# Kernel tuning notes

Measured on AMD Instinct MI355X. Metric: run time of the kernel, lower is better.

The kernel has to match this reference:

```python
import jax, jax.numpy as jnp
import numpy as np

N = 100000
F_IN = 128
HID = 64
N_CLS = 40
E = 1600000


def gcn_conv(x, src, dst, W, b, n_nodes):
    """PyG GCNConv: add self-loops, symmetric deg^{-1/2} normalization.

    Self-loop contribution handled analytically (norm_ii = 1/deg_i) so we
    never concatenate self-loop edges.
    """
    h = x @ W                                      # [N, out]
    # in-degree including self-loop
    deg = jax.ops.segment_sum(jnp.ones((src.shape[0],), x.dtype), dst,
                              num_segments=n_nodes) + 1.0
    dinv = jax.lax.rsqrt(deg)                      # deg^{-1/2}, [N]
    norm = dinv[src] * dinv[dst]                   # [E]
    msg = h[src] * norm[:, None]                   # [E, out] gather + scale
    agg = jax.ops.segment_sum(msg, dst, num_segments=n_nodes)
    return agg + h * (dinv * dinv)[:, None] + b


def setup_inputs() -> dict:
    key = jax.random.key(0)
    k1, k2, k3, k4, k5, k6 = jax.random.split(key, 6)
    x = jax.random.normal(k1, (N, F_IN), dtype=jnp.float32)
    edge_index = jax.random.randint(k2, (2, E), 0, N, dtype=jnp.int64)
    W1 = jax.random.normal(k3, (F_IN, HID), dtype=jnp.float32) / np.sqrt(F_IN)
    b1 = jnp.zeros((HID,), jnp.float32)
    W2 = jax.random.normal(k4, (HID, N_CLS), dtype=jnp.float32) / np.sqrt(HID)
    b2 = jnp.zeros((N_CLS,), jnp.float32)
    return {"x": x, "edge_index": edge_index, "W1": W1, "b1": b1,
            "W2": W2, "b2": b2}


def reference(x, edge_index, W1, b1, W2, b2):
    src, dst = edge_index[0], edge_index[1]
    h = jax.nn.relu(gcn_conv(x, src, dst, W1, b1, N))
    # dropout p=0.5 is identity at inference (training=False)
    out = gcn_conv(h, src, dst, W2, b2, N)
    return out
```

## Files before the change

kernel.cpp:

```cpp
#include <hip/hip_runtime.h>
#include <stdint.h>

#define NN    100000
#define FIN   128
#define HIDN  64
#define NCLS  40
#define NE    1600000
#define NBUCK ((NN + 255) / 256)
#define EPB   4096
#define NEB   ((NE + EPB - 1) / EPB)

typedef unsigned int uint32;
typedef __attribute__((ext_vector_type(8))) short short8v;
typedef __attribute__((ext_vector_type(4))) float f32x4;

static __device__ __forceinline__ unsigned short f2bf(float f) {
  uint32 u = __float_as_uint(f);
  u = (u + 0x7fffu + ((u >> 16) & 1u)) >> 16;
  return (unsigned short)u;
}
static __device__ __forceinline__ uint32 pack2(float lo, float hi) {
  return (uint32)f2bf(lo) | ((uint32)f2bf(hi) << 16);
}
static __device__ __forceinline__ float bf_lo(uint32 v) {
  return __uint_as_float(v << 16);
}
static __device__ __forceinline__ float bf_hi(uint32 v) {
  return __uint_as_float(v & 0xFFFF0000u);
}
static __device__ __forceinline__ f32x4 mfma_bf16(uint4 a, uint4 b, f32x4 c) {
  short8v av = __builtin_bit_cast(short8v, a);
  short8v bv = __builtin_bit_cast(short8v, b);
  return __builtin_amdgcn_mfma_f32_16x16x32_bf16(av, bv, c, 0, 0, 0);
}

static __device__ __forceinline__ int perm_col(int z) {
  return 4 * (z >> 3) + ((z & 7) >> 1) + 16 * (z & 1) + ((z >= 32) ? 16 : 0);
}

__global__ __launch_bounds__(64) void probe_kernel(const unsigned int* __restrict__ raw,
                                                   int* __restrict__ flag) {
  if (threadIdx.x == 0) {
    int is64 = 1;
    for (int i = 0; i < 64; ++i)
      if (raw[2 * i + 1] != 0u) { is64 = 0; break; }
    *flag = is64;
  }
}

__global__ __launch_bounds__(64) void wfrag_kernel(const float* __restrict__ W,
                                                   const float* __restrict__ b1,
                                                   uint4* __restrict__ wfrag,
                                                   float* __restrict__ b1p) {
  int idx = blockIdx.x * 64 + threadIdx.x;
  if (idx < 64) b1p[idx] = b1[perm_col(idx)];
  int lane = idx & 63;
  int nr = (idx >> 6) & 3;
  int kr = (idx >> 8) & 3;
  int t  = idx >> 10;
  int n  = nr * 16 + (lane & 15);
  int k0 = kr * 32 + (lane >> 4) * 8;
  uint32 w[4];
#pragma unroll
  for (int j = 0; j < 4; ++j) {
    float a = W[(k0 + 2 * j) * HIDN + n];
    float b = W[(k0 + 2 * j + 1) * HIDN + n];
    uint32 ha = f2bf(a), hb = f2bf(b);
    if (t == 0) {
      w[j] = ha | (hb << 16);
    } else {
      float ra = a - __uint_as_float(ha << 16);
      float rb = b - __uint_as_float(hb << 16);
      w[j] = (uint32)f2bf(ra) | ((uint32)f2bf(rb) << 16);
    }
  }
  wfrag[idx] = make_uint4(w[0], w[1], w[2], w[3]);
}

__global__ __launch_bounds__(256) void passA_kernel(const void* __restrict__ eptr,
                                                    const int* __restrict__ flag,
                                                    int* __restrict__ mat) {
  __shared__ int cnt[NBUCK];
  int tid = threadIdx.x;
  for (int i = tid; i < NBUCK; i += 256) cnt[i] = 0;
  __syncthreads();
  int is64 = *flag;
  int base = blockIdx.x * EPB;
#pragma unroll
  for (int k = 0; k < EPB / 256; ++k) {
    int e = base + k * 256 + tid;
    if (e < NE) {
      int d = is64 ? (int)((const long long*)eptr)[e + NE]
                   : ((const int*)eptr)[e + NE];
      atomicAdd(&cnt[d >> 8], 1);
    }
  }
  __syncthreads();
  for (int i = tid; i < NBUCK; i += 256)
    mat[blockIdx.x * NBUCK + i] = cnt[i];
}

__global__ __launch_bounds__(512) void passB1_kernel(int* __restrict__ mat,
                                                     int* __restrict__ tot) {
  __shared__ int s[512];
  int b = blockIdx.x;
  int t = threadIdx.x;
  int v = (t < NEB) ? mat[t * NBUCK + b] : 0;
  s[t] = v;
  __syncthreads();
#pragma unroll
  for (int d = 1; d < 512; d <<= 1) {
    int u = (t >= d) ? s[t - d] : 0;
    __syncthreads();
    s[t] += u;
    __syncthreads();
  }
  if (t < NEB) mat[t * NBUCK + b] = s[t] - v;
  if (t == 511) tot[b] = s[511];
}

__global__ __launch_bounds__(512) void passB2_kernel(const int* __restrict__ tot,
                                                     int* __restrict__ bbase) {
  __shared__ int s[512];
  int i = threadIdx.x;
  int v = (i < NBUCK) ? tot[i] : 0;
  s[i] = v;
  __syncthreads();
#pragma unroll
  for (int d = 1; d < 512; d <<= 1) {
    int u = (i >= d) ? s[i - d] : 0;
    __syncthreads();
    s[i] += u;
    __syncthreads();
  }
  if (i < NBUCK) bbase[i] = s[i] - v;
  if (i == 511) bbase[NBUCK] = s[511];
}

__global__ __launch_bounds__(256) void passC_kernel(const void* __restrict__ eptr,
                                                    const int* __restrict__ flag,
                                                    const int* __restrict__ mat,
                                                    const int* __restrict__ bbase,
                                                    uint32* __restrict__ bbuf) {
  __shared__ int cur[NBUCK];
  int tid = threadIdx.x;
  for (int i = tid; i < NBUCK; i += 256)
    cur[i] = bbase[i] + mat[blockIdx.x * NBUCK + i];
  __syncthreads();
  int is64 = *flag;
  int base = blockIdx.x * EPB;
#pragma unroll
  for (int k = 0; k < EPB / 256; ++k) {
    int e = base + k * 256 + tid;
    if (e < NE) {
      int s, d;
      if (is64) {
        const long long* p = (const long long*)eptr;
        s = (int)p[e]; d = (int)p[e + NE];
      } else {
        const int* p = (const int*)eptr;
        s = p[e]; d = p[e + NE];
      }
      int slot = atomicAdd(&cur[d >> 8], 1);
      bbuf[slot] = (uint32)s | ((uint32)(d & 255) << 17);
    }
  }
}

__global__ __launch_bounds__(256) void build_kernel(const int* __restrict__ bbase,
                                                    const uint32* __restrict__ bbuf,
                                                    int* __restrict__ off,
                                                    float* __restrict__ dinv,
                                                    int* __restrict__ s_src) {
  __shared__ int hist[256];
  __shared__ int lofs[256];
  __shared__ int rank[256];
  int b = blockIdx.x, tid = threadIdx.x;
  int base = bbase[b];
  int count = bbase[b + 1] - base;
  const uint32* p = bbuf + base;
  hist[tid] = 0;
  __syncthreads();
  for (int i = tid; i < count; i += 256) atomicAdd(&hist[p[i] >> 17], 1);
  __syncthreads();
  int deg = hist[tid];
  lofs[tid] = deg;
  __syncthreads();
#pragma unroll
  for (int dd = 1; dd < 256; dd <<= 1) {
    int t = (tid >= dd) ? lofs[tid - dd] : 0;
    __syncthreads();
    lofs[tid] += t;
    __syncthreads();
  }
  int excl = lofs[tid] - deg;
  __syncthreads();
  lofs[tid] = excl;
  rank[tid] = 0;
  int n = b * 256 + tid;
  if (n < NN) {
    off[n] = base + excl;
    dinv[n] = rsqrtf((float)deg + 1.0f);
  }
  if (b == 0 && tid == 0) off[NN] = NE;
  __syncthreads();
  for (int i = tid; i < count; i += 256) {
    uint32 v = p[i];
    int dl = (int)(v >> 17);
    int s = (int)(v & 0x1FFFFu);
    int r = atomicAdd(&rank[dl], 1);
    s_src[base + lofs[dl] + r] = s;
  }
}

__global__ __launch_bounds__(256) void gemm1_kernel(const float* __restrict__ x,
                                                    const uint4* __restrict__ wfrag,
                                                    const float* __restrict__ dinv,
                                                    uint32* __restrict__ hs) {
  int wid = blockIdx.x * 4 + (threadIdx.x >> 6);
  if (wid >= NN / 32) return;
  int lane = threadIdx.x & 63;
  int l15 = lane & 15, lg = lane >> 4;
  int r0 = wid * 32;
  f32x4 acc[2][4];
#pragma unroll
  for (int mr = 0; mr < 2; ++mr)
#pragma unroll
    for (int nr = 0; nr < 4; ++nr) acc[mr][nr] = (f32x4)0.f;
  const float4* x4 = (const float4*)x;
#pragma unroll
  for (int kr = 0; kr < 4; ++kr) {
    uint4 ah[2], al[2];
#pragma unroll
    for (int mr = 0; mr < 2; ++mr) {
      int m = r0 + mr * 16 + l15;
      int q0 = m * 32 + kr * 8 + lg * 2;
      float4 u = x4[q0], v = x4[q0 + 1];
      float xs[8] = {u.x, u.y, u.z, u.w, v.x, v.y, v.z, v.w};
      uint32 hw[4], lw[4];
#pragma unroll
      for (int j = 0; j < 4; ++j) {
        float a0 = xs[2 * j], a1 = xs[2 * j + 1];
        uint32 h0 = f2bf(a0), h1 = f2bf(a1);
        float ra = a0 - __uint_as_float(h0 << 16);
        float rb = a1 - __uint_as_float(h1 << 16);
        hw[j] = h0 | (h1 << 16);
        lw[j] = (uint32)f2bf(ra) | ((uint32)f2bf(rb) << 16);
      }
      ah[mr] = make_uint4(hw[0], hw[1], hw[2], hw[3]);
      al[mr] = make_uint4(lw[0], lw[1], lw[2], lw[3]);
    }
#pragma unroll
    for (int nr = 0; nr < 4; ++nr) {
      uint4 bh = wfrag[(kr * 4 + nr) * 64 + lane];
      uint4 bl = wfrag[((4 + kr) * 4 + nr) * 64 + lane];
#pragma unroll
      for (int mr = 0; mr < 2; ++mr) {
        acc[mr][nr] = mfma_bf16(ah[mr], bh, acc[mr][nr]);
        acc[mr][nr] = mfma_bf16(al[mr], bh, acc[mr][nr]);
        acc[mr][nr] = mfma_bf16(ah[mr], bl, acc[mr][nr]);
      }
    }
  }
#pragma unroll
  for (int mr = 0; mr < 2; ++mr) {
    int rb = r0 + mr * 16 + 4 * lg;
    float4 dv = *(const float4*)&dinv[rb];
#pragma unroll
    for (int a = 0; a < 2; ++a) {
#pragma unroll
      for (int j = 0; j < 4; ++j) {
        float d = (&dv.x)[j];
        uint32 wv = pack2(acc[mr][2 * a][j] * d, acc[mr][2 * a + 1][j] * d);
        hs[(size_t)(rb + j) * 32 + a * 16 + l15] = wv;
      }
    }
  }
}

__global__ __launch_bounds__(256) void agg1_kernel(const int* __restrict__ off,
                                                   const int* __restrict__ s_src,
                                                   const uint4* __restrict__ hs4,
                                                   const float* __restrict__ dinv,
                                                   const float* __restrict__ b1p,
                                                   uint4* __restrict__ g) {
  int tid = threadIdx.x;
  int n = blockIdx.x * 32 + (tid >> 3);
  int hc = tid & 7;
  int j0 = off[n], j1 = off[n + 1];
  float a[8];
  {
    uint4 v = hs4[(size_t)n * 8 + hc];
    a[0] = bf_lo(v.x); a[1] = bf_hi(v.x); a[2] = bf_lo(v.y); a[3] = bf_hi(v.y);
    a[4] = bf_lo(v.z); a[5] = bf_hi(v.z); a[6] = bf_lo(v.w); a[7] = bf_hi(v.w);
  }
  int j = j0;
  for (; j + 1 < j1; j += 2) {
    int sa = s_src[j], sb = s_src[j + 1];
    uint4 va = hs4[(size_t)sa * 8 + hc];
    uint4 vb = hs4[(size_t)sb * 8 + hc];
    a[0] += bf_lo(va.x); a[1] += bf_hi(va.x); a[2] += bf_lo(va.y); a[3] += bf_hi(va.y);
    a[4] += bf_lo(va.z); a[5] += bf_hi(va.z); a[6] += bf_lo(va.w); a[7] += bf_hi(va.w);
    a[0] += bf_lo(vb.x); a[1] += bf_hi(vb.x); a[2] += bf_lo(vb.y); a[3] += bf_hi(vb.y);
    a[4] += bf_lo(vb.z); a[5] += bf_hi(vb.z); a[6] += bf_lo(vb.w); a[7] += bf_hi(vb.w);
  }
  if (j < j1) {
    int sa = s_src[j];
    uint4 va = hs4[(size_t)sa * 8 + hc];
    a[0] += bf_lo(va.x); a[1] += bf_hi(va.x); a[2] += bf_lo(va.y); a[3] += bf_hi(va.y);
    a[4] += bf_lo(va.z); a[5] += bf_hi(va.z); a[6] += bf_lo(va.w); a[7] += bf_hi(va.w);
  }
  float di = dinv[n];
  float4 b0 = *(const float4*)&b1p[hc * 8];
  float4 b4 = *(const float4*)&b1p[hc * 8 + 4];
  float r0 = di * fmaxf(a[0] * di + b0.x, 0.f);
  float r1 = di * fmaxf(a[1] * di + b0.y, 0.f);
  float r2 = di * fmaxf(a[2] * di + b0.z, 0.f);
  float r3 = di * fmaxf(a[3] * di + b0.w, 0.f);
  float r4 = di * fmaxf(a[4] * di + b4.x, 0.f);
  float r5 = di * fmaxf(a[5] * di + b4.y, 0.f);
  float r6 = di * fmaxf(a[6] * di + b4.z, 0.f);
  float r7 = di * fmaxf(a[7] * di + b4.w, 0.f);
  uint4 o;
  o.x = pack2(r0, r1); o.y = pack2(r2, r3);
  o.z = pack2(r4, r5); o.w = pack2(r6, r7);
  g[(size_t)n * 8 + hc] = o;
}

__global__ __launch_bounds__(256) void agg2_kernel(const int* __restrict__ off,
                                                   const int* __restrict__ s_src,
                                                   const uint4* __restrict__ g,
                                                   const float* __restrict__ dinv,
                                                   float* __restrict__ t) {
  int tid = threadIdx.x;
  int n = blockIdx.x * 32 + (tid >> 3);
  int hc = tid & 7;
  int j0 = off[n], j1 = off[n + 1];
  float a[8];
  {
    uint4 v = g[(size_t)n * 8 + hc];
    a[0] = bf_lo(v.x); a[1] = bf_hi(v.x); a[2] = bf_lo(v.y); a[3] = bf_hi(v.y);
    a[4] = bf_lo(v.z); a[5] = bf_hi(v.z); a[6] = bf_lo(v.w); a[7] = bf_hi(v.w);
  }
  int j = j0;
  for (; j + 1 < j1; j += 2) {
    int sa = s_src[j], sb = s_src[j + 1];
    uint4 va = g[(size_t)sa * 8 + hc];
    uint4 vb = g[(size_t)sb * 8 + hc];
    a[0] += bf_lo(va.x); a[1] += bf_hi(va.x); a[2] += bf_lo(va.y); a[3] += bf_hi(va.y);
    a[4] += bf_lo(va.z); a[5] += bf_hi(va.z); a[6] += bf_lo(va.w); a[7] += bf_hi(va.w);
    a[0] += bf_lo(vb.x); a[1] += bf_hi(vb.x); a[2] += bf_lo(vb.y); a[3] += bf_hi(vb.y);
    a[4] += bf_lo(vb.z); a[5] += bf_hi(vb.z); a[6] += bf_lo(vb.w); a[7] += bf_hi(vb.w);
  }
  if (j < j1) {
    int sa = s_src[j];
    uint4 va = g[(size_t)sa * 8 + hc];
    a[0] += bf_lo(va.x); a[1] += bf_hi(va.x); a[2] += bf_lo(va.y); a[3] += bf_hi(va.y);
    a[4] += bf_lo(va.z); a[5] += bf_hi(va.z); a[6] += bf_lo(va.w); a[7] += bf_hi(va.w);
  }
  float di = dinv[n];
  float* tp = &t[(size_t)n * HIDN + hc * 8];
  *(float4*)tp = make_float4(a[0] * di, a[1] * di, a[2] * di, a[3] * di);
  *(float4*)(tp + 4) = make_float4(a[4] * di, a[5] * di, a[6] * di, a[7] * di);
}

__global__ __launch_bounds__(256) void mv_kernel(const float* __restrict__ t,
                                                 const float* __restrict__ W2,
                                                 const float* __restrict__ b2,
                                                 float* __restrict__ out) {
  __shared__ float sW[HIDN * NCLS];
  int tid = threadIdx.x;
  for (int i = tid; i < HIDN * (NCLS / 4); i += 256) {
    int z = i / 10, j = i - z * 10;
    int c = perm_col(z);
    ((float4*)sW)[z * 10 + j] = ((const float4*)W2)[c * 10 + j];
  }
  __syncthreads();
  int cg = tid & 1;
  int r = blockIdx.x * 128 + (tid >> 1);
  if (r >= NN) return;
  int c0 = cg * 20;
  float acc[20];
#pragma unroll
  for (int j = 0; j < 20; ++j) acc[j] = b2[c0 + j];
  const float4* t4 = (const float4*)(t + (size_t)r * HIDN);
#pragma unroll 4
  for (int k4 = 0; k4 < 16; ++k4) {
    float4 tv = t4[k4];
#pragma unroll
    for (int kk = 0; kk < 4; ++kk) {
      float xv = (&tv.x)[kk];
      const float* wr = &sW[(k4 * 4 + kk) * NCLS + c0];
#pragma unroll
      for (int j = 0; j < 5; ++j) {
        float4 wv = *(const float4*)&wr[j * 4];
        acc[j * 4 + 0] = fmaf(xv, wv.x, acc[j * 4 + 0]);
        acc[j * 4 + 1] = fmaf(xv, wv.y, acc[j * 4 + 1]);
        acc[j * 4 + 2] = fmaf(xv, wv.z, acc[j * 4 + 2]);
        acc[j * 4 + 3] = fmaf(xv, wv.w, acc[j * 4 + 3]);
      }
    }
  }
  float4* op = (float4*)&out[(size_t)r * NCLS + c0];
#pragma unroll
  for (int j = 0; j < 5; ++j)
    op[j] = make_float4(acc[j * 4 + 0], acc[j * 4 + 1],
                        acc[j * 4 + 2], acc[j * 4 + 3]);
}

extern "C" void kernel_launch(void* const* d_in, const int* in_sizes, int n_in,
                              void* d_out, int out_size, void* d_ws, size_t ws_size,
                              hipStream_t stream) {
  const float* x  = (const float*)d_in[0];
  const void*  ei = d_in[1];
  const float* W1 = (const float*)d_in[2];
  const float* b1 = (const float*)d_in[3];
  const float* W2 = (const float*)d_in[4];
  const float* b2 = (const float*)d_in[5];
  float* out = (float*)d_out;

  char* w = (char*)d_ws;
  size_t off_b = 0;
  auto carve = [&](size_t bytes) -> void* {
    void* p = w + off_b;
    off_b = (off_b + bytes + 255) & ~(size_t)255;
    return p;
  };
  int*    mat   = (int*)   carve((size_t)NEB * NBUCK * 4);
  int*    tot   = (int*)   carve((size_t)NBUCK * 4);
  int*    bbase = (int*)   carve((size_t)(NBUCK + 1) * 4);
  int*    offs  = (int*)   carve((size_t)(NN + 1) * 4);
  float*  dinv  = (float*) carve((size_t)NN * 4);
  int*    flag  = (int*)   carve(256);
  int*    s_src = (int*)   carve((size_t)NE * 4);
  uint32* hs    = (uint32*)carve((size_t)NN * 32 * 4);
  uint4*  g     = (uint4*) carve((size_t)NN * 8 * 16);
  float*  t     = (float*) carve((size_t)NN * HIDN * 4);
  uint32* bbuf  = (uint32*)carve((size_t)NE * 4);
  uint4*  wfrag = (uint4*) carve((size_t)2048 * 16);
  float*  b1p   = (float*) carve((size_t)HIDN * 4);

  probe_kernel<<<1, 64, 0, stream>>>((const unsigned int*)ei, flag);
  wfrag_kernel<<<32, 64, 0, stream>>>(W1, b1, wfrag, b1p);
  passA_kernel<<<NEB, 256, 0, stream>>>(ei, flag, mat);
  passB1_kernel<<<NBUCK, 512, 0, stream>>>(mat, tot);
  passB2_kernel<<<1, 512, 0, stream>>>(tot, bbase);
  passC_kernel<<<NEB, 256, 0, stream>>>(ei, flag, mat, bbase, bbuf);
  build_kernel<<<NBUCK, 256, 0, stream>>>(bbase, bbuf, offs, dinv, s_src);
  gemm1_kernel<<<(NN / 32 + 3) / 4, 256, 0, stream>>>(x, wfrag, dinv, hs);
  agg1_kernel<<<NN / 32, 256, 0, stream>>>(offs, s_src, (const uint4*)hs, dinv, b1p, g);
  agg2_kernel<<<NN / 32, 256, 0, stream>>>(offs, s_src, g, dinv, t);
  mv_kernel<<<(NN + 127) / 128, 256, 0, stream>>>(t, W2, b2, out);
}
```

Measured before the change: 247.1 us.

## Fuse second aggregation with W2 matvec via LDS and unroll gathers by four

Merges the layer-2 aggregation and the final 64x40 matvec into one kernel. Each block stages its 32 aggregated rows in shared memory, then every thread computes 5 output classes using a transposed, column-permuted W2 that is prepared once in the weight prep kernel. This removes the fp32 intermediate t round trip through global memory (about 25.6 MB written and read) and one launch. Both aggregation loops now unroll neighbor gathers by four to keep more loads in flight. The trade-off is that W2 is read from global/L2 per thread rather than from LDS, and output stores are scalar and strided.

New measurement: 334.7 us. 35.4% more time.

```diff
diff --git a/kernel.cpp b/kernel.cpp
--- a/kernel.cpp
+++ b/kernel.cpp
@@ -38,6 +38,14 @@
   return 4 * (z >> 3) + ((z & 7) >> 1) + 16 * (z & 1) + ((z >= 32) ? 16 : 0);
 }
 
+#define ACC8(v)                                                              \
+  do {                                                                       \
+    a[0] += bf_lo((v).x); a[1] += bf_hi((v).x);                              \
+    a[2] += bf_lo((v).y); a[3] += bf_hi((v).y);                              \
+    a[4] += bf_lo((v).z); a[5] += bf_hi((v).z);                              \
+    a[6] += bf_lo((v).w); a[7] += bf_hi((v).w);                              \
+  } while (0)
+
 __global__ __launch_bounds__(64) void probe_kernel(const unsigned int* __restrict__ raw,
                                                    int* __restrict__ flag) {
   if (threadIdx.x == 0) {
@@ -50,10 +58,16 @@
 
 __global__ __launch_bounds__(64) void wfrag_kernel(const float* __restrict__ W,
                                                    const float* __restrict__ b1,
+                                                   const float* __restrict__ W2,
                                                    uint4* __restrict__ wfrag,
-                                                   float* __restrict__ b1p) {
+                                                   float* __restrict__ b1p,
+                                                   float* __restrict__ W2pc) {
   int idx = blockIdx.x * 64 + threadIdx.x;
   if (idx < 64) b1p[idx] = b1[perm_col(idx)];
+  for (int i = idx; i < HIDN * NCLS; i += 2048) {
+    int c = i >> 6, z = i & 63;
+    W2pc[i] = W2[perm_col(z) * NCLS + c];
+  }
   int lane = idx & 63;
   int nr = (idx >> 6) & 3;
   int kr = (idx >> 8) & 3;
@@ -295,20 +309,17 @@
     a[4] = bf_lo(v.z); a[5] = bf_hi(v.z); a[6] = bf_lo(v.w); a[7] = bf_hi(v.w);
   }
   int j = j0;
-  for (; j + 1 < j1; j += 2) {
-    int sa = s_src[j], sb = s_src[j + 1];
-    uint4 va = hs4[(size_t)sa * 8 + hc];
-    uint4 vb = hs4[(size_t)sb * 8 + hc];
-    a[0] += bf_lo(va.x); a[1] += bf_hi(va.x); a[2] += bf_lo(va.y); a[3] += bf_hi(va.y);
-    a[4] += bf_lo(va.z); a[5] += bf_hi(va.z); a[6] += bf_lo(va.w); a[7] += bf_hi(va.w);
-    a[0] += bf_lo(vb.x); a[1] += bf_hi(vb.x); a[2] += bf_lo(vb.y); a[3] += bf_hi(vb.y);
-    a[4] += bf_lo(vb.z); a[5] += bf_hi(vb.z); a[6] += bf_lo(vb.w); a[7] += bf_hi(vb.w);
-  }
-  if (j < j1) {
-    int sa = s_src[j];
-    uint4 va = hs4[(size_t)sa * 8 + hc];
-    a[0] += bf_lo(va.x); a[1] += bf_hi(va.x); a[2] += bf_lo(va.y); a[3] += bf_hi(va.y);
-    a[4] += bf_lo(va.z); a[5] += bf_hi(va.z); a[6] += bf_lo(va.w); a[7] += bf_hi(va.w);
+  for (; j + 3 < j1; j += 4) {
+    int s0 = s_src[j], s1 = s_src[j + 1], s2 = s_src[j + 2], s3 = s_src[j + 3];
+    uint4 v0 = hs4[(size_t)s0 * 8 + hc];
+    uint4 v1 = hs4[(size_t)s1 * 8 + hc];
+    uint4 v2 = hs4[(size_t)s2 * 8 + hc];
+    uint4 v3 = hs4[(size_t)s3 * 8 + hc];
+    ACC8(v0); ACC8(v1); ACC8(v2); ACC8(v3);
+  }
+  for (; j < j1; ++j) {
+    uint4 v0 = hs4[(size_t)s_src[j] * 8 + hc];
+    ACC8(v0);
   }
   float di = dinv[n];
   float4 b0 = *(const float4*)&b1p[hc * 8];
@@ -327,13 +338,17 @@
   g[(size_t)n * 8 + hc] = o;
 }
 
-__global__ __launch_bounds__(256) void agg2_kernel(const int* __restrict__ off,
-                                                   const int* __restrict__ s_src,
-                                                   const uint4* __restrict__ g,
-                                                   const float* __restrict__ dinv,
-                                                   float* __restrict__ t) {
+__global__ __launch_bounds__(256) void agg2mv_kernel(const int* __restrict__ off,
+                                                     const int* __restrict__ s_src,
+                                                     const uint4* __restrict__ g,
+                                                     const float* __restrict__ dinv,
+                                                     const float* __restrict__ W2pc,
+                                                     const float* __restrict__ b2,
+                                                     float* __restrict__ out) {
+  __shared__ float t_lds[32 * 68];
   int tid = threadIdx.x;
-  int n = blockIdx.x * 32 + (tid >> 3);
+  int node = tid >> 3;
+  int n = blockIdx.x * 32 + node;
   int hc = tid & 7;
   int j0 = off[n], j1 = off[n + 1];
   float a[8];
@@ -343,69 +358,45 @@
     a[4] = bf_lo(v.z); a[5] = bf_hi(v.z); a[6] = bf_lo(v.w); a[7] = bf_hi(v.w);
   }
   int j = j0;
-  for (; j + 1 < j1; j += 2) {
-    int sa = s_src[j], sb = s_src[j + 1];
-    uint4 va = g[(size_t)sa * 8 + hc];
-    uint4 vb = g[(size_t)sb * 8 + hc];
-    a[0] += bf_lo(va.x); a[1] += bf_hi(va.x); a[2] += bf_lo(va.y); a[3] += bf_hi(va.y);
-    a[4] += bf_lo(va.z); a[5] += bf_hi(va.z); a[6] += bf_lo(va.w); a[7] += bf_hi(va.w);
-    a[0] += bf_lo(vb.x); a[1] += bf_hi(vb.x); a[2] += bf_lo(vb.y); a[3] += bf_hi(vb.y);
-    a[4] += bf_lo(vb.z); a[5] += bf_hi(vb.z); a[6] += bf_lo(vb.w); a[7] += bf_hi(vb.w);
-  }
-  if (j < j1) {
-    int sa = s_src[j];
-    uint4 va = g[(size_t)sa * 8 + hc];
-    a[0] += bf_lo(va.x); a[1] += bf_hi(va.x); a[2] += bf_lo(va.y); a[3] += bf_hi(va.y);
-    a[4] += bf_lo(va.z); a[5] += bf_hi(va.z); a[6] += bf_lo(va.w); a[7] += bf_hi(va.w);
+  for (; j + 3 < j1; j += 4) {
+    int s0 = s_src[j], s1 = s_src[j + 1], s2 = s_src[j + 2], s3 = s_src[j + 3];
+    uint4 v0 = g[(size_t)s0 * 8 + hc];
+    uint4 v1 = g[(size_t)s1 * 8 + hc];
+    uint4 v2 = g[(size_t)s2 * 8 + hc];
+    uint4 v3 = g[(size_t)s3 * 8 + hc];
+    ACC8(v0); ACC8(v1); ACC8(v2); ACC8(v3);
+  }
+  for (; j < j1; ++j) {
+    uint4 v0 = g[(size_t)s_src[j] * 8 + hc];
+    ACC8(v0);
   }
   float di = dinv[n];
-  float* tp = &t[(size_t)n * HIDN + hc * 8];
-  *(float4*)tp = make_float4(a[0] * di, a[1] * di, a[2] * di, a[3] * di);
-  *(float4*)(tp + 4) = make_float4(a[4] * di, a[5] * di, a[6] * di, a[7] * di);
-}
-
-__global__ __launch_bounds__(256) void mv_kernel(const float* __restrict__ t,
-                                                 const float* __restrict__ W2,
-                                                 const float* __restrict__ b2,
-                                                 float* __restrict__ out) {
-  __shared__ float sW[HIDN * NCLS];
-  int tid = threadIdx.x;
-  for (int i = tid; i < HIDN * (NCLS / 4); i += 256) {
-    int z = i / 10, j = i - z * 10;
-    int c = perm_col(z);
-    ((float4*)sW)[z * 10 + j] = ((const float4*)W2)[c * 10 + j];
-  }
-  __syncthreads();
-  int cg = tid & 1;
-  int r = blockIdx.x * 128 + (tid >> 1);
-  if (r >= NN) return;
-  int c0 = cg * 20;
-  float acc[20];
-#pragma unroll
-  for (int j = 0; j < 20; ++j) acc[j] = b2[c0 + j];
-  const float4* t4 = (const float4*)(t + (size_t)r * HIDN);
-#pragma unroll 4
-  for (int k4 = 0; k4 < 16; ++k4) {
-    float4 tv = t4[k4];
-#pragma unroll
-    for (int kk = 0; kk < 4; ++kk) {
-      float xv = (&tv.x)[kk];
-      const float* wr = &sW[(k4 * 4 + kk) * NCLS + c0];
-#pragma unroll
-      for (int j = 0; j < 5; ++j) {
-        float4 wv = *(const float4*)&wr[j * 4];
-        acc[j * 4 + 0] = fmaf(xv, wv.x, acc[j * 4 + 0]);
-        acc[j * 4 + 1] = fmaf(xv, wv.y, acc[j * 4 + 1]);
-        acc[j * 4 + 2] = fmaf(xv, wv.z, acc[j * 4 + 2]);
-        acc[j * 4 + 3] = fmaf(xv, wv.w, acc[j * 4 + 3]);
-      }
-    }
-  }
-  float4* op = (float4*)&out[(size_t)r * NCLS + c0];
-#pragma unroll
-  for (int j = 0; j < 5; ++j)
-    op[j] = make_float4(acc[j * 4 + 0], acc[j * 4 + 1],
-                        acc[j * 4 + 2], acc[j * 4 + 3]);
+  {
+    float* tp = &t_lds[node * 68 + hc * 8];
+    ((float4*)tp)[0] = make_float4(a[0] * di, a[1] * di, a[2] * di, a[3] * di);
+    ((float4*)tp)[1] = make_float4(a[4] * di, a[5] * di, a[6] * di, a[7] * di);
+  }
+  __syncthreads();
+  int c0 = hc * 5;
+  float acc5[5];
+#pragma unroll
+  for (int c = 0; c < 5; ++c) acc5[c] = b2[c0 + c];
+  const float4* tl = (const float4*)&t_lds[node * 68];
+  const float4* W2pc4 = (const float4*)W2pc;
+#pragma unroll
+  for (int z4 = 0; z4 < 16; ++z4) {
+    float4 tv = tl[z4];
+#pragma unroll
+    for (int c = 0; c < 5; ++c) {
+      float4 wv = W2pc4[(c0 + c) * 16 + z4];
+      acc5[c] = fmaf(tv.x, wv.x, acc5[c]);
+      acc5[c] = fmaf(tv.y, wv.y, acc5[c]);
+      acc5[c] = fmaf(tv.z, wv.z, acc5[c]);
+      acc5[c] = fmaf(tv.w, wv.w, acc5[c]);
+    }
+  }
+#pragma unroll
+  for (int c = 0; c < 5; ++c) out[(size_t)n * NCLS + c0 + c] = acc5[c];
 }
 
 extern "C" void kernel_launch(void* const* d_in, const int* in_sizes, int n_in,
@@ -435,13 +426,13 @@
   int*    s_src = (int*)   carve((size_t)NE * 4);
   uint32* hs    = (uint32*)carve((size_t)NN * 32 * 4);
   uint4*  g     = (uint4*) carve((size_t)NN * 8 * 16);
-  float*  t     = (float*) carve((size_t)NN * HIDN * 4);
   uint32* bbuf  = (uint32*)carve((size_t)NE * 4);
   uint4*  wfrag = (uint4*) carve((size_t)2048 * 16);
   float*  b1p   = (float*) carve((size_t)HIDN * 4);
+  float*  W2pc  = (float*) carve((size_t)HIDN * NCLS * 4);
 
   probe_kernel<<<1, 64, 0, stream>>>((const unsigned int*)ei, flag);
-  wfrag_kernel<<<32, 64, 0, stream>>>(W1, b1, wfrag, b1p);
+  wfrag_kernel<<<32, 64, 0, stream>>>(W1, b1, W2, wfrag, b1p, W2pc);
   passA_kernel<<<NEB, 256, 0, stream>>>(ei, flag, mat);
   passB1_kernel<<<NBUCK, 512, 0, stream>>>(mat, tot);
   passB2_kernel<<<1, 512, 0, stream>>>(tot, bbase);
@@ -449,6 +440,5 @@
   build_kernel<<<NBUCK, 256, 0, stream>>>(bbase, bbuf, offs, dinv, s_src);
   gemm1_kernel<<<(NN / 32 + 3) / 4, 256, 0, stream>>>(x, wfrag, dinv, hs);
   agg1_kernel<<<NN / 32, 256, 0, stream>>>(offs, s_src, (const uint4*)hs, dinv, b1p, g);
-  agg2_kernel<<<NN / 32, 256, 0, stream>>>(offs, s_src, g, dinv, t);
-  mv_kernel<<<(NN + 127) / 128, 256, 0, stream>>>(t, W2, b2, out);
-}
+  agg2mv_kernel<<<NN / 32, 256, 0, stream>>>(offs, s_src, g, dinv, W2pc, b2, out);
+}
```
